# Kernel optimization log

Measured on AMD Instinct MI355X. Metric: run time of the kernel, lower is better.

## Reference

```python
import jax, jax.numpy as jnp
import numpy as np

B, N, F_IN, F_E, H, L = 8, 128, 64, 16, 256, 8
EPS = 1e-5


def _linear_params(key, fan_in, fan_out):
    k1, k2 = jax.random.split(key)
    bound = 1.0 / np.sqrt(fan_in)
    W = jax.random.uniform(k1, (fan_in, fan_out), minval=-bound, maxval=bound, dtype=jnp.float32)
    b = jax.random.uniform(k2, (fan_out,), minval=-bound, maxval=bound, dtype=jnp.float32)
    return W, b


def setup_inputs() -> dict:
    key = jax.random.key(0)
    ks = jax.random.split(key, 16)
    x = jax.random.normal(ks[0], (B, N, F_IN), dtype=jnp.float32)
    adj = jax.random.randint(ks[1], (B, N, N), 0, 2, dtype=jnp.int32)
    edge_attr = jax.random.normal(ks[2], (B, N, N, F_E), dtype=jnp.float32)
    mask = jnp.ones((B, N), dtype=jnp.int32)

    node_W, node_b = _linear_params(ks[3], F_IN, H)
    edge_W, edge_b = _linear_params(ks[4], F_E, H)

    lks = jax.random.split(ks[5], L)
    W1s, b1s, W2s, b2s = [], [], [], []
    for i in range(L):
        a, b_ = jax.random.split(lks[i])
        W1, b1 = _linear_params(a, H, H)
        W2, b2 = _linear_params(b_, H, H)
        W1s.append(W1); b1s.append(b1); W2s.append(W2); b2s.append(b2)
    ln_g = jnp.ones((L, H), dtype=jnp.float32)
    ln_b = jnp.zeros((L, H), dtype=jnp.float32)
    W1 = jnp.stack(W1s); b1 = jnp.stack(b1s)
    W2 = jnp.stack(W2s); b2 = jnp.stack(b2s)

    ro_pW, ro_pb = _linear_params(ks[6], H, H)
    ro_aW, ro_ab = _linear_params(ks[7], H, 1)
    ph_W, ph_b = _linear_params(ks[8], H, 1)

    return dict(x=x, adj=adj, edge_attr=edge_attr, mask=mask,
                node_W=node_W, node_b=node_b, edge_W=edge_W, edge_b=edge_b,
                ln_g=ln_g, ln_b=ln_b, W1=W1, b1=b1, W2=W2, b2=b2,
                ro_pW=ro_pW, ro_pb=ro_pb, ro_aW=ro_aW, ro_ab=ro_ab,
                ph_W=ph_W, ph_b=ph_b)


def _layernorm(x, g, b):
    mu = jnp.mean(x, axis=-1, keepdims=True)
    var = jnp.var(x, axis=-1, keepdims=True)
    return (x - mu) * jax.lax.rsqrt(var + EPS) * g + b


def _gine_forward(x, adjf, edge_attr, maskf,
                  node_W, node_b, edge_W, edge_b,
                  ln_g, ln_b, W1, b1, W2, b2,
                  ro_pW, ro_pb, ro_aW, ro_ab, ph_W, ph_b):
    h = x @ node_W + node_b                      # (B,N,H)
    edge_emb = edge_attr @ edge_W + edge_b       # (B,N,N,H)
    m = maskf[..., None]                         # (B,N,1)

    def layer(h, p):
        g, bln, w1, bb1, w2, bb2 = p
        h = h * m
        h_norm = _layernorm(h, g, bln)
        # message: h_j + e_ij, j indexes axis 2 -> broadcast over axis 1
        m_in = h_norm[:, None, :, :] + edge_emb          # (B,N,N,H)
        mm = jax.nn.relu(jax.nn.relu(m_in @ w1 + bb1) @ w2 + bb2)
        mm = mm * adjf[..., None]
        msg = mm.sum(axis=2)                             # (B,N,H)
        out = (h + msg) * m
        return out, None

    h, _ = jax.lax.scan(layer, h, (ln_g, ln_b, W1, b1, W2, b2))

    # attention readout
    hp = jnp.tanh(h @ ro_pW + ro_pb)
    scores = (hp @ ro_aW).squeeze(-1) + ro_ab            # (B,N)
    scores = jnp.where(maskf > 0, scores, -jnp.inf)
    alpha = jax.nn.softmax(scores, axis=1)
    cnt = jnp.clip(maskf.sum(axis=1, keepdims=True), 1.0, None)
    fallback = jnp.where(maskf > 0, 1.0 / cnt, 0.0)
    alpha = jnp.where(jnp.isnan(alpha), fallback, alpha)
    gvec = (h * alpha[..., None]).sum(axis=1)            # (B,H)
    out = (gvec @ ph_W + ph_b).squeeze(-1)               # (B,)
    return out


def reference(x, adj, edge_attr, mask,
              node_W, node_b, edge_W, edge_b,
              ln_g, ln_b, W1, b1, W2, b2,
              ro_pW, ro_pb, ro_aW, ro_ab, ph_W, ph_b):
    adjf = adj.astype(jnp.float32)
    maskf = mask.astype(jnp.float32)
    return _gine_forward(x, adjf, edge_attr, maskf,
                         node_W, node_b, edge_W, edge_b,
                         ln_g, ln_b, W1, b1, W2, b2,
                         ro_pW, ro_pb, ro_aW, ro_ab, ph_W, ph_b)
```

## Files before the change

kernel.cpp:

```cpp
#include <hip/hip_runtime.h>

typedef float  f32x4  __attribute__((ext_vector_type(4)));
typedef short  bf16x8 __attribute__((ext_vector_type(8)));
typedef unsigned short u16;
typedef unsigned int   u32;

static __device__ __forceinline__ u16 f2bf(float f) {
    u32 u = __float_as_uint(f);
    u += 0x7FFFu + ((u >> 16) & 1u);
    return (u16)(u >> 16);
}



__global__ void k_h0(const float* __restrict__ x, const float* __restrict__ nW,
                     const float* __restrict__ nb, float* __restrict__ h) {
    __shared__ float xr[64];
    int row = blockIdx.x, c = threadIdx.x;
    if (c < 64) xr[c] = x[row * 64 + c];
    __syncthreads();
    float acc = nb[c];
#pragma unroll
    for (int k = 0; k < 64; ++k) acc += xr[k] * nW[k * 256 + c];
    h[row * 256 + c] = acc;
}

__global__ void k_edgefrag(const float* __restrict__ ea, u16* __restrict__ ef) {
    int gid = blockIdx.x * 256 + threadIdx.x;
    int lane = gid & 63, nt = (gid >> 6) & 7, i = (gid >> 9) & 127, b = gid >> 16;
    int j = nt * 16 + (lane & 15), k0 = (lane >> 4) * 8;
    uint4 out = {0u, 0u, 0u, 0u};
    if (k0 < 16) {
        const float* p = ea + (((size_t)(b * 128 + i) * 128 + j) * 16 + k0);
        u16 us[8];
#pragma unroll
        for (int t = 0; t < 8; ++t) us[t] = f2bf(p[t]);
        out.x = (u32)us[0] | ((u32)us[1] << 16);
        out.y = (u32)us[2] | ((u32)us[3] << 16);
        out.z = (u32)us[4] | ((u32)us[5] << 16);
        out.w = (u32)us[6] | ((u32)us[7] << 16);
    }
    ((uint4*)ef)[gid] = out;
}

__global__ void k_wt(const float* __restrict__ W1, const float* __restrict__ W2,
                     u16* __restrict__ w1t, u16* __restrict__ w2t) {
    int gid = blockIdx.x * 256 + threadIdx.x;
    int lane = gid & 63, mt = (gid >> 6) & 15, kt = (gid >> 10) & 7, l = gid >> 13;
    int hh = mt * 16 + (lane & 15), k = kt * 32 + (lane >> 4) * 8;
    u16 a[8], b[8];
#pragma unroll
    for (int t = 0; t < 8; ++t) {
        size_t idx = (size_t)l * 65536 + (size_t)(k + t) * 256 + hh;
        a[t] = f2bf(W1[idx]);
        b[t] = f2bf(W2[idx]);
    }
    uint4 oa, ob;
    oa.x = (u32)a[0] | ((u32)a[1] << 16); oa.y = (u32)a[2] | ((u32)a[3] << 16);
    oa.z = (u32)a[4] | ((u32)a[5] << 16); oa.w = (u32)a[6] | ((u32)a[7] << 16);
    ob.x = (u32)b[0] | ((u32)b[1] << 16); ob.y = (u32)b[2] | ((u32)b[3] << 16);
    ob.z = (u32)b[4] | ((u32)b[5] << 16); ob.w = (u32)b[6] | ((u32)b[7] << 16);
    ((uint4*)w1t)[gid] = oa;
    ((uint4*)w2t)[gid] = ob;
}

__global__ void k_wf1b(const float* __restrict__ eW, const float* __restrict__ eb,
                       const float* __restrict__ W1, const float* __restrict__ b1,
                       u16* __restrict__ wf, float* __restrict__ bias1) {
    __shared__ float eWsT[256 * 16];
    __shared__ float ebS[256];
    int l = blockIdx.x, tid = threadIdx.x;
#pragma unroll
    for (int k = 0; k < 16; ++k) eWsT[tid * 16 + k] = eW[k * 256 + tid];
    ebS[tid] = eb[tid];
    __syncthreads();
    float acc[16];
#pragma unroll
    for (int k = 0; k < 16; ++k) acc[k] = 0.f;
    float bacc = b1[l * 256 + tid];
    const float* w1c = W1 + (size_t)l * 65536 + tid;
    for (int c = 0; c < 256; ++c) {
        float wv = w1c[(size_t)c * 256];
        const f32x4* e = (const f32x4*)&eWsT[c * 16];
#pragma unroll
        for (int q = 0; q < 4; ++q) {
            f32x4 ev = e[q];
#pragma unroll
            for (int t = 0; t < 4; ++t) acc[q * 4 + t] += ev[t] * wv;
        }
        bacc += ebS[c] * wv;
    }
    bias1[l * 256 + tid] = bacc;
    int mt = tid >> 4, lo = tid & 15;
#pragma unroll
    for (int c4 = 0; c4 < 4; ++c4) {
        u16 us[8];
#pragma unroll
        for (int t = 0; t < 8; ++t) {
            int k = c4 * 8 + t;
            us[t] = (k < 16) ? f2bf(acc[k]) : (u16)0;
        }
        uint4 o;
        o.x = (u32)us[0] | ((u32)us[1] << 16);
        o.y = (u32)us[2] | ((u32)us[3] << 16);
        o.z = (u32)us[4] | ((u32)us[5] << 16);
        o.w = (u32)us[6] | ((u32)us[7] << 16);
        ((uint4*)wf)[(size_t)(l * 16 + mt) * 64 + c4 * 16 + lo] = o;
    }
}


__global__ void k_ln(float* __restrict__ h, const int* __restrict__ mask,
                     const float* __restrict__ lng, const float* __restrict__ lnb,
                     u16* __restrict__ hnbf) {
    __shared__ float rs[4], rs2[4];
    int row = blockIdx.x, c = threadIdx.x;
    float mv = (float)mask[row];
    float v = h[row * 256 + c] * mv;
    h[row * 256 + c] = v;
    float s = v, s2 = v * v;
    int w = c >> 6, lane = c & 63;
#pragma unroll
    for (int off = 32; off; off >>= 1) {
        s  += __shfl_xor(s,  off);
        s2 += __shfl_xor(s2, off);
    }
    if (lane == 0) { rs[w] = s; rs2[w] = s2; }
    __syncthreads();
    float S  = rs[0] + rs[1] + rs[2] + rs[3];
    float S2 = rs2[0] + rs2[1] + rs2[2] + rs2[3];
    float mu  = S * (1.f / 256.f);
    float var = S2 * (1.f / 256.f) - mu * mu;
    float rstd = rsqrtf(var + 1e-5f);
    hnbf[row * 256 + c] = f2bf((v - mu) * rstd * lng[c] + lnb[c]);
}

__global__ __launch_bounds__(256) void k_hn1(const u16* __restrict__ w1t,
        const u16* __restrict__ hnbf, const float* __restrict__ bias1,
        float* __restrict__ hn1p, int l) {
    int orig = blockIdx.x;
    int bid = (orig & 7) * 8 + (orig >> 3);
    int b = bid >> 3, q = bid & 7;
    int tid = threadIdx.x, w = tid >> 6, lane = tid & 63;
    int mt = q * 2 + (w >> 1), nb_ = (w & 1) * 4;
    f32x4 bv = *(const f32x4*)(bias1 + l * 256 + mt * 16 + (lane >> 4) * 4);
    f32x4 acc[4];
#pragma unroll
    for (int n = 0; n < 4; ++n) acc[n] = bv;
#pragma unroll
    for (int kt = 0; kt < 8; ++kt) {
        bf16x8 a = *(const bf16x8*)(w1t + ((size_t)((l * 8 + kt) * 16 + mt) * 64 + lane) * 8);
#pragma unroll
        for (int nn = 0; nn < 4; ++nn) {
            int j = (nb_ + nn) * 16 + (lane & 15);
            bf16x8 bt = *(const bf16x8*)(hnbf + ((size_t)(b * 128 + j) * 256 + kt * 32 + (lane >> 4) * 8));
            acc[nn] = __builtin_amdgcn_mfma_f32_16x16x32_bf16(a, bt, acc[nn], 0, 0, 0);
        }
    }
    float* outb = hn1p + (size_t)b * 32768;
#pragma unroll
    for (int nn = 0; nn < 4; ++nn)
        *(f32x4*)(outb + ((size_t)(mt * 8 + nb_ + nn) * 64 + lane) * 4) = acc[nn];
}

__global__ __launch_bounds__(512, 4) void k_msg(
        const u16* __restrict__ wf1t, const u16* __restrict__ ef,
        const u16* __restrict__ w2t,  const float* __restrict__ hn1p,
        const float* __restrict__ b2, const int* __restrict__ adj,
        const int* __restrict__ mask, float* __restrict__ h,
        const float* __restrict__ lngN, const float* __restrict__ lnbN,
        u16* __restrict__ hnbf, int l, int doLN) {

    __shared__ __align__(16) u16  t1S[8 * 8 * 64 * 8];
    __shared__ __align__(16) float adjS[128];
    __shared__ __align__(16) float b2S[256];
    __shared__ __align__(16) float msgS[256];
    __shared__ float rs[8], rs2[8];

    int orig = blockIdx.x;
    int bid = (orig & 7) * 128 + (orig >> 3);
    int b = bid >> 7, i = bid & 127;
    int tid = threadIdx.x, w = tid >> 6, lane = tid & 63;
    int row = b * 128 + i;

    if (tid < 128) adjS[tid] = (float)adj[(size_t)row * 128 + tid];
    if (tid < 256) b2S[tid] = b2[l * 256 + tid];

    const u16* efb = ef + (size_t)row * 4096;
    bf16x8 be[8];
#pragma unroll
    for (int n = 0; n < 8; ++n)
        be[n] = *(const bf16x8*)(efb + (n * 64 + lane) * 8);

    const float* hpb = hn1p + (size_t)b * 32768;
#pragma unroll
    for (int m = 0; m < 2; ++m) {
        int mt = w * 2 + m;
        bf16x8 a = *(const bf16x8*)(wf1t + ((size_t)(l * 16 + mt) * 64 + lane) * 8);
#pragma unroll
        for (int n = 0; n < 8; ++n) {
            f32x4 acc = *(const f32x4*)(hpb + ((size_t)(mt * 8 + n) * 64 + lane) * 4);
            acc = __builtin_amdgcn_mfma_f32_16x16x32_bf16(a, be[n], acc, 0, 0, 0);
            u32 lo = (u32)f2bf(fmaxf(acc[0], 0.f)) | ((u32)f2bf(fmaxf(acc[1], 0.f)) << 16);
            u32 hi = (u32)f2bf(fmaxf(acc[2], 0.f)) | ((u32)f2bf(fmaxf(acc[3], 0.f)) << 16);
            int g    = ((mt & 1) << 1) | (lane >> 5);
            int half = (lane >> 4) & 1;
            uint2 pk; pk.x = lo; pk.y = hi;
            *(uint2*)(t1S + ((size_t)(((mt >> 1) * 8 + n) * 64) + g * 16 + (lane & 15)) * 8 + half * 4) = pk;
        }
    }
    __syncthreads();

    f32x4 acc2[2][8];
#pragma unroll
    for (int m = 0; m < 2; ++m)
#pragma unroll
        for (int n = 0; n < 8; ++n) acc2[m][n] = (f32x4){0.f, 0.f, 0.f, 0.f};

#pragma unroll
    for (int kt = 0; kt < 8; ++kt) {
        bf16x8 a2[2];
#pragma unroll
        for (int m = 0; m < 2; ++m)
            a2[m] = *(const bf16x8*)(w2t + ((size_t)((l * 8 + kt) * 16 + (w * 2 + m)) * 64 + lane) * 8);
#pragma unroll
        for (int n = 0; n < 8; ++n) {
            bf16x8 bt = *(const bf16x8*)(t1S + ((size_t)(kt * 8 + n) * 64 + lane) * 8);
#pragma unroll
            for (int m = 0; m < 2; ++m)
                acc2[m][n] = __builtin_amdgcn_mfma_f32_16x16x32_bf16(a2[m], bt, acc2[m][n], 0, 0, 0);
        }
    }

#pragma unroll
    for (int m = 0; m < 2; ++m) {
        int hb = (w * 2 + m) * 16 + (lane >> 4) * 4;
        f32x4 bv = *(const f32x4*)(&b2S[hb]);
        f32x4 ms = (f32x4){0.f, 0.f, 0.f, 0.f};
#pragma unroll
        for (int n = 0; n < 8; ++n) {
            float aw = adjS[n * 16 + (lane & 15)];
#pragma unroll
            for (int r = 0; r < 4; ++r)
                ms[r] += fmaxf(acc2[m][n][r] + bv[r], 0.f) * aw;
        }
#pragma unroll
        for (int r = 0; r < 4; ++r) {
            ms[r] += __shfl_xor(ms[r], 1);
            ms[r] += __shfl_xor(ms[r], 2);
            ms[r] += __shfl_xor(ms[r], 4);
            ms[r] += __shfl_xor(ms[r], 8);
        }
        if ((lane & 15) == 0) *(f32x4*)(&msgS[hb]) = ms;
    }
    __syncthreads();

    float v = 0.f;
    if (tid < 256) {
        float mv = (float)mask[row];
        v = (h[(size_t)row * 256 + tid] + msgS[tid]) * mv;
        h[(size_t)row * 256 + tid] = v;
    }
    float s = v, s2 = v * v;
#pragma unroll
    for (int off = 32; off; off >>= 1) {
        s  += __shfl_xor(s,  off);
        s2 += __shfl_xor(s2, off);
    }
    if (lane == 0) { rs[w] = s; rs2[w] = s2; }
    __syncthreads();
    if (doLN && tid < 256) {
        float S = 0.f, S2 = 0.f;
#pragma unroll
        for (int t = 0; t < 8; ++t) { S += rs[t]; S2 += rs2[t]; }
        float mu  = S * (1.f / 256.f);
        float var = S2 * (1.f / 256.f) - mu * mu;
        float rstd = rsqrtf(var + 1e-5f);
        hnbf[(size_t)row * 256 + tid] = f2bf((v - mu) * rstd * lngN[tid] + lnbN[tid]);
    }
}


__global__ void k_ro1(const float* __restrict__ h, const float* __restrict__ pW,
                      const float* __restrict__ pb, const float* __restrict__ aW,
                      const float* __restrict__ ab, float* __restrict__ scores) {
    __shared__ float hr[8][256];
    __shared__ float red[4][8];
    int blk = blockIdx.x, b = blk >> 4, g = blk & 15;
    int tid = threadIdx.x;
    size_t base = (size_t)(b * 128 + g * 8) * 256;
#pragma unroll
    for (int t = 0; t < 8; ++t) hr[t][tid] = h[base + t * 256 + tid];
    __syncthreads();
    float facc[8];
    float pbv = pb[tid];
#pragma unroll
    for (int j = 0; j < 8; ++j) facc[j] = pbv;
    for (int k = 0; k < 256; ++k) {
        float wv = pW[(size_t)k * 256 + tid];
#pragma unroll
        for (int j = 0; j < 8; ++j) facc[j] += hr[j][k] * wv;
    }
    float awc = aW[tid];
    int w = tid >> 6, lane = tid & 63;
#pragma unroll
    for (int j = 0; j < 8; ++j) {
        float v = tanhf(facc[j]) * awc;
#pragma unroll
        for (int off = 32; off; off >>= 1) v += __shfl_xor(v, off);
        if (lane == 0) red[w][j] = v;
    }
    __syncthreads();
    if (tid < 8)
        scores[b * 128 + g * 8 + tid] = red[0][tid] + red[1][tid] + red[2][tid] + red[3][tid] + ab[0];
}

__global__ void k_ro2(const float* __restrict__ h, const float* __restrict__ scores,
                      const int* __restrict__ mask, const float* __restrict__ phW,
                      const float* __restrict__ phb, float* __restrict__ out) {
    __shared__ float aS[128];
    __shared__ float rm[4], rc[4], red[4];
    int b = blockIdx.x, tid = threadIdx.x, w = tid >> 6, lane = tid & 63;
    float mv = 0.f, sv = -__builtin_inff();
    if (tid < 128) {
        mv = (float)mask[b * 128 + tid];
        if (mv > 0.f) sv = scores[b * 128 + tid];
    }
    float mx = sv, cs = mv;
#pragma unroll
    for (int off = 32; off; off >>= 1) {
        mx = fmaxf(mx, __shfl_xor(mx, off));
        cs += __shfl_xor(cs, off);
    }
    if (lane == 0) { rm[w] = mx; rc[w] = cs; }
    __syncthreads();
    mx = fmaxf(fmaxf(rm[0], rm[1]), fmaxf(rm[2], rm[3]));
    float cnt = rc[0] + rc[1] + rc[2] + rc[3];
    float e = (tid < 128 && mv > 0.f) ? expf(sv - mx) : 0.f;
    float se = e;
#pragma unroll
    for (int off = 32; off; off >>= 1) se += __shfl_xor(se, off);
    if (lane == 0) red[w] = se;
    __syncthreads();
    float S = red[0] + red[1] + red[2] + red[3];
    if (tid < 128) {
        float a;
        if (S > 0.f) a = e / S;
        else         a = (mv > 0.f) ? 1.f / fmaxf(cnt, 1.f) : 0.f;
        aS[tid] = a;
    }
    __syncthreads();
    float g = 0.f;
    const float* hb = h + (size_t)b * 128 * 256;
    for (int n = 0; n < 128; ++n) g += aS[n] * hb[(size_t)n * 256 + tid];
    float p = g * phW[tid];
#pragma unroll
    for (int off = 32; off; off >>= 1) p += __shfl_xor(p, off);
    __syncthreads();
    if (lane == 0) red[w] = p;
    __syncthreads();
    if (tid == 0) out[b] = red[0] + red[1] + red[2] + red[3] + phb[0];
}

extern "C" void kernel_launch(void* const* d_in, const int* in_sizes, int n_in,
                              void* d_out, int out_size, void* d_ws, size_t ws_size,
                              hipStream_t stream) {
    const float* x    = (const float*)d_in[0];
    const int*   adj  = (const int*)  d_in[1];
    const float* ea   = (const float*)d_in[2];
    const int*   mask = (const int*)  d_in[3];
    const float* nW   = (const float*)d_in[4];
    const float* nb   = (const float*)d_in[5];
    const float* eW   = (const float*)d_in[6];
    const float* eb   = (const float*)d_in[7];
    const float* lng  = (const float*)d_in[8];
    const float* lnb  = (const float*)d_in[9];
    const float* W1   = (const float*)d_in[10];
    const float* b1   = (const float*)d_in[11];
    const float* W2   = (const float*)d_in[12];
    const float* b2   = (const float*)d_in[13];
    const float* ropW = (const float*)d_in[14];
    const float* ropb = (const float*)d_in[15];
    const float* roaW = (const float*)d_in[16];
    const float* roab = (const float*)d_in[17];
    const float* phW  = (const float*)d_in[18];
    const float* phb  = (const float*)d_in[19];
    float* out = (float*)d_out;

    char* p = (char*)d_ws;
    auto alloc = [&](size_t bytes) { char* r = p; p += (bytes + 255) & ~(size_t)255; return r; };
    float* h     = (float*)alloc((size_t)8 * 128 * 256 * 4);
    u16*   hnbf  = (u16*)  alloc((size_t)8 * 128 * 256 * 2);
    float* hn1p  = (float*)alloc((size_t)8 * 32768 * 4);
    u16*   ef    = (u16*)  alloc((size_t)8 * 128 * 4096 * 2);
    u16*   wf1t  = (u16*)  alloc((size_t)8 * 16 * 64 * 8 * 2);
    u16*   w1t   = (u16*)  alloc((size_t)8 * 8 * 16 * 64 * 8 * 2);
    u16*   w2t   = (u16*)  alloc((size_t)8 * 8 * 16 * 64 * 8 * 2);
    float* bias1 = (float*)alloc((size_t)8 * 256 * 4);
    float* scores= (float*)alloc((size_t)1024 * 4);

    k_h0      <<<1024, 256, 0, stream>>>(x, nW, nb, h);
    k_edgefrag<<<2048, 256, 0, stream>>>(ea, ef);
    k_wt      <<<256,  256, 0, stream>>>(W1, W2, w1t, w2t);
    k_wf1b    <<<8,    256, 0, stream>>>(eW, eb, W1, b1, wf1t, bias1);
    k_ln      <<<1024, 256, 0, stream>>>(h, mask, lng, lnb, hnbf);

    for (int l = 0; l < 8; ++l) {
        k_hn1<<<64,   256, 0, stream>>>(w1t, hnbf, bias1, hn1p, l);
        int doLN = (l < 7) ? 1 : 0;
        int ln_next = (l < 7) ? (l + 1) : l;
        k_msg<<<1024, 512, 0, stream>>>(wf1t, ef, w2t, hn1p, b2, adj, mask, h,
                                        lng + ln_next * 256, lnb + ln_next * 256,
                                        hnbf, l, doLN);
    }

    k_ro1<<<128, 256, 0, stream>>>(h, ropW, ropb, roaW, roab, scores);
    k_ro2<<<8,   256, 0, stream>>>(h, scores, mask, phW, phb, out);
}
```

Baseline: 396.3 us.

## Compact adjacency neighbors and skip MLP work on absent edges

After: 355.8 us. -10.2%, faster.

```diff
diff --git a/kernel.cpp b/kernel.cpp
--- a/kernel.cpp
+++ b/kernel.cpp
@@ -13,16 +13,36 @@
 
 
 
-__global__ void k_h0(const float* __restrict__ x, const float* __restrict__ nW,
-                     const float* __restrict__ nb, float* __restrict__ h) {
+__global__ void k_h0ln(const float* __restrict__ x, const float* __restrict__ nW,
+                       const float* __restrict__ nb, const int* __restrict__ mask,
+                       const float* __restrict__ lng, const float* __restrict__ lnb,
+                       float* __restrict__ h, u16* __restrict__ hnbf) {
     __shared__ float xr[64];
+    __shared__ float rs[4], rs2[4];
     int row = blockIdx.x, c = threadIdx.x;
     if (c < 64) xr[c] = x[row * 64 + c];
     __syncthreads();
     float acc = nb[c];
 #pragma unroll
     for (int k = 0; k < 64; ++k) acc += xr[k] * nW[k * 256 + c];
-    h[row * 256 + c] = acc;
+    float mv = (float)mask[row];
+    float v = acc * mv;
+    h[row * 256 + c] = v;
+    float s = v, s2 = v * v;
+    int w = c >> 6, lane = c & 63;
+#pragma unroll
+    for (int off = 32; off; off >>= 1) {
+        s  += __shfl_xor(s,  off);
+        s2 += __shfl_xor(s2, off);
+    }
+    if (lane == 0) { rs[w] = s; rs2[w] = s2; }
+    __syncthreads();
+    float S  = rs[0] + rs[1] + rs[2] + rs[3];
+    float S2 = rs2[0] + rs2[1] + rs2[2] + rs2[3];
+    float mu  = S * (1.f / 256.f);
+    float var = S2 * (1.f / 256.f) - mu * mu;
+    float rstd = rsqrtf(var + 1e-5f);
+    hnbf[row * 256 + c] = f2bf((v - mu) * rstd * lng[c] + lnb[c]);
 }
 
 __global__ void k_edgefrag(const float* __restrict__ ea, u16* __restrict__ ef) {
@@ -110,57 +130,27 @@
 }
 
 
-__global__ void k_ln(float* __restrict__ h, const int* __restrict__ mask,
-                     const float* __restrict__ lng, const float* __restrict__ lnb,
-                     u16* __restrict__ hnbf) {
-    __shared__ float rs[4], rs2[4];
-    int row = blockIdx.x, c = threadIdx.x;
-    float mv = (float)mask[row];
-    float v = h[row * 256 + c] * mv;
-    h[row * 256 + c] = v;
-    float s = v, s2 = v * v;
-    int w = c >> 6, lane = c & 63;
-#pragma unroll
-    for (int off = 32; off; off >>= 1) {
-        s  += __shfl_xor(s,  off);
-        s2 += __shfl_xor(s2, off);
-    }
-    if (lane == 0) { rs[w] = s; rs2[w] = s2; }
-    __syncthreads();
-    float S  = rs[0] + rs[1] + rs[2] + rs[3];
-    float S2 = rs2[0] + rs2[1] + rs2[2] + rs2[3];
-    float mu  = S * (1.f / 256.f);
-    float var = S2 * (1.f / 256.f) - mu * mu;
-    float rstd = rsqrtf(var + 1e-5f);
-    hnbf[row * 256 + c] = f2bf((v - mu) * rstd * lng[c] + lnb[c]);
-}
-
 __global__ __launch_bounds__(256) void k_hn1(const u16* __restrict__ w1t,
         const u16* __restrict__ hnbf, const float* __restrict__ bias1,
         float* __restrict__ hn1p, int l) {
     int orig = blockIdx.x;
-    int bid = (orig & 7) * 8 + (orig >> 3);
-    int b = bid >> 3, q = bid & 7;
+    int bid = (orig & 7) * 16 + (orig >> 3);
+    int b = bid >> 4, mt = bid & 15;
     int tid = threadIdx.x, w = tid >> 6, lane = tid & 63;
-    int mt = q * 2 + (w >> 1), nb_ = (w & 1) * 4;
     f32x4 bv = *(const f32x4*)(bias1 + l * 256 + mt * 16 + (lane >> 4) * 4);
-    f32x4 acc[4];
-#pragma unroll
-    for (int n = 0; n < 4; ++n) acc[n] = bv;
+    f32x4 acc0 = bv, acc1 = bv;
+    int j0 = (w * 2) * 16 + (lane & 15), j1 = j0 + 16;
 #pragma unroll
     for (int kt = 0; kt < 8; ++kt) {
         bf16x8 a = *(const bf16x8*)(w1t + ((size_t)((l * 8 + kt) * 16 + mt) * 64 + lane) * 8);
-#pragma unroll
-        for (int nn = 0; nn < 4; ++nn) {
-            int j = (nb_ + nn) * 16 + (lane & 15);
-            bf16x8 bt = *(const bf16x8*)(hnbf + ((size_t)(b * 128 + j) * 256 + kt * 32 + (lane >> 4) * 8));
-            acc[nn] = __builtin_amdgcn_mfma_f32_16x16x32_bf16(a, bt, acc[nn], 0, 0, 0);
-        }
+        bf16x8 bt0 = *(const bf16x8*)(hnbf + ((size_t)(b * 128 + j0) * 256 + kt * 32 + (lane >> 4) * 8));
+        bf16x8 bt1 = *(const bf16x8*)(hnbf + ((size_t)(b * 128 + j1) * 256 + kt * 32 + (lane >> 4) * 8));
+        acc0 = __builtin_amdgcn_mfma_f32_16x16x32_bf16(a, bt0, acc0, 0, 0, 0);
+        acc1 = __builtin_amdgcn_mfma_f32_16x16x32_bf16(a, bt1, acc1, 0, 0, 0);
     }
     float* outb = hn1p + (size_t)b * 32768;
-#pragma unroll
-    for (int nn = 0; nn < 4; ++nn)
-        *(f32x4*)(outb + ((size_t)(mt * 8 + nb_ + nn) * 64 + lane) * 4) = acc[nn];
+    *(f32x4*)(outb + ((size_t)(mt * 8 + w * 2) * 64 + lane) * 4)     = acc0;
+    *(f32x4*)(outb + ((size_t)(mt * 8 + w * 2 + 1) * 64 + lane) * 4) = acc1;
 }
 
 __global__ __launch_bounds__(512, 4) void k_msg(
@@ -172,9 +162,11 @@
         u16* __restrict__ hnbf, int l, int doLN) {
 
     __shared__ __align__(16) u16  t1S[8 * 8 * 64 * 8];
-    __shared__ __align__(16) float adjS[128];
     __shared__ __align__(16) float b2S[256];
     __shared__ __align__(16) float msgS[256];
+    __shared__ int listS[128];
+    __shared__ int flagS[128];
+    __shared__ int cntS;
     __shared__ float rs[8], rs2[8];
 
     int orig = blockIdx.x;
@@ -183,75 +175,92 @@
     int tid = threadIdx.x, w = tid >> 6, lane = tid & 63;
     int row = b * 128 + i;
 
-    if (tid < 128) adjS[tid] = (float)adj[(size_t)row * 128 + tid];
+    if (tid < 128) { flagS[tid] = adj[(size_t)row * 128 + tid]; listS[tid] = 0; }
     if (tid < 256) b2S[tid] = b2[l * 256 + tid];
-
-    const u16* efb = ef + (size_t)row * 4096;
-    bf16x8 be[8];
-#pragma unroll
-    for (int n = 0; n < 8; ++n)
-        be[n] = *(const bf16x8*)(efb + (n * 64 + lane) * 8);
-
+    __syncthreads();
+
+    if (w == 0) {
+        int f0 = flagS[lane], f1 = flagS[64 + lane];
+        unsigned long long m0 = __ballot(f0 != 0);
+        unsigned long long m1 = __ballot(f1 != 0);
+        unsigned long long lt = (1ull << lane) - 1ull;
+        int c0 = __popcll(m0);
+        if (f0) listS[__popcll(m0 & lt)] = lane;
+        if (f1) listS[c0 + __popcll(m1 & lt)] = 64 + lane;
+        if (lane == 0) cntS = c0 + __popcll(m1);
+    }
+    __syncthreads();
+    int cnt = cntS;
+    int NT = (cnt + 15) >> 4;
+
+    const u16*  efb = ef + (size_t)row * 4096;
     const float* hpb = hn1p + (size_t)b * 32768;
-#pragma unroll
-    for (int m = 0; m < 2; ++m) {
-        int mt = w * 2 + m;
-        bf16x8 a = *(const bf16x8*)(wf1t + ((size_t)(l * 16 + mt) * 64 + lane) * 8);
-#pragma unroll
-        for (int n = 0; n < 8; ++n) {
-            f32x4 acc = *(const f32x4*)(hpb + ((size_t)(mt * 8 + n) * 64 + lane) * 4);
-            acc = __builtin_amdgcn_mfma_f32_16x16x32_bf16(a, be[n], acc, 0, 0, 0);
+    int mt0 = w * 2, mt1 = w * 2 + 1;
+    bf16x8 aG0 = *(const bf16x8*)(wf1t + ((size_t)(l * 16 + mt0) * 64 + lane) * 8);
+    bf16x8 aG1 = *(const bf16x8*)(wf1t + ((size_t)(l * 16 + mt1) * 64 + lane) * 8);
+    for (int n = 0; n < NT; ++n) {
+        int j = listS[n * 16 + (lane & 15)];
+        int jo = (j >> 4) * 64 + (lane & 48) + (j & 15);
+        bf16x8 be = *(const bf16x8*)(efb + (size_t)jo * 8);
+        {
+            f32x4 ci = *(const f32x4*)(hpb + ((size_t)(mt0 * 8) * 64 + jo) * 4);
+            f32x4 acc = __builtin_amdgcn_mfma_f32_16x16x32_bf16(aG0, be, ci, 0, 0, 0);
             u32 lo = (u32)f2bf(fmaxf(acc[0], 0.f)) | ((u32)f2bf(fmaxf(acc[1], 0.f)) << 16);
             u32 hi = (u32)f2bf(fmaxf(acc[2], 0.f)) | ((u32)f2bf(fmaxf(acc[3], 0.f)) << 16);
-            int g    = ((mt & 1) << 1) | (lane >> 5);
-            int half = (lane >> 4) & 1;
+            int g = ((mt0 & 1) << 1) | (lane >> 5), half = (lane >> 4) & 1;
             uint2 pk; pk.x = lo; pk.y = hi;
-            *(uint2*)(t1S + ((size_t)(((mt >> 1) * 8 + n) * 64) + g * 16 + (lane & 15)) * 8 + half * 4) = pk;
-        }
-    }
-    __syncthreads();
-
-    f32x4 acc2[2][8];
-#pragma unroll
-    for (int m = 0; m < 2; ++m)
-#pragma unroll
-        for (int n = 0; n < 8; ++n) acc2[m][n] = (f32x4){0.f, 0.f, 0.f, 0.f};
-
+            *(uint2*)(t1S + ((size_t)((w * 8 + n) * 64) + g * 16 + (lane & 15)) * 8 + half * 4) = pk;
+        }
+        {
+            f32x4 ci = *(const f32x4*)(hpb + ((size_t)(mt1 * 8) * 64 + jo) * 4);
+            f32x4 acc = __builtin_amdgcn_mfma_f32_16x16x32_bf16(aG1, be, ci, 0, 0, 0);
+            u32 lo = (u32)f2bf(fmaxf(acc[0], 0.f)) | ((u32)f2bf(fmaxf(acc[1], 0.f)) << 16);
+            u32 hi = (u32)f2bf(fmaxf(acc[2], 0.f)) | ((u32)f2bf(fmaxf(acc[3], 0.f)) << 16);
+            int g = ((mt1 & 1) << 1) | (lane >> 5), half = (lane >> 4) & 1;
+            uint2 pk; pk.x = lo; pk.y = hi;
+            *(uint2*)(t1S + ((size_t)((w * 8 + n) * 64) + g * 16 + (lane & 15)) * 8 + half * 4) = pk;
+        }
+    }
+    __syncthreads();
+
+    bf16x8 a2[8][2];
 #pragma unroll
     for (int kt = 0; kt < 8; ++kt) {
-        bf16x8 a2[2];
-#pragma unroll
-        for (int m = 0; m < 2; ++m)
-            a2[m] = *(const bf16x8*)(w2t + ((size_t)((l * 8 + kt) * 16 + (w * 2 + m)) * 64 + lane) * 8);
-#pragma unroll
-        for (int n = 0; n < 8; ++n) {
+        a2[kt][0] = *(const bf16x8*)(w2t + ((size_t)((l * 8 + kt) * 16 + mt0) * 64 + lane) * 8);
+        a2[kt][1] = *(const bf16x8*)(w2t + ((size_t)((l * 8 + kt) * 16 + mt1) * 64 + lane) * 8);
+    }
+    int hb0 = mt0 * 16 + (lane >> 4) * 4;
+    int hb1 = mt1 * 16 + (lane >> 4) * 4;
+    f32x4 bv0 = *(const f32x4*)(&b2S[hb0]);
+    f32x4 bv1 = *(const f32x4*)(&b2S[hb1]);
+    f32x4 ms0 = (f32x4){0.f, 0.f, 0.f, 0.f};
+    f32x4 ms1 = (f32x4){0.f, 0.f, 0.f, 0.f};
+    for (int n = 0; n < NT; ++n) {
+        f32x4 acc0 = (f32x4){0.f, 0.f, 0.f, 0.f};
+        f32x4 acc1 = (f32x4){0.f, 0.f, 0.f, 0.f};
+#pragma unroll
+        for (int kt = 0; kt < 8; ++kt) {
             bf16x8 bt = *(const bf16x8*)(t1S + ((size_t)(kt * 8 + n) * 64 + lane) * 8);
-#pragma unroll
-            for (int m = 0; m < 2; ++m)
-                acc2[m][n] = __builtin_amdgcn_mfma_f32_16x16x32_bf16(a2[m], bt, acc2[m][n], 0, 0, 0);
-        }
-    }
-
-#pragma unroll
-    for (int m = 0; m < 2; ++m) {
-        int hb = (w * 2 + m) * 16 + (lane >> 4) * 4;
-        f32x4 bv = *(const f32x4*)(&b2S[hb]);
-        f32x4 ms = (f32x4){0.f, 0.f, 0.f, 0.f};
-#pragma unroll
-        for (int n = 0; n < 8; ++n) {
-            float aw = adjS[n * 16 + (lane & 15)];
-#pragma unroll
-            for (int r = 0; r < 4; ++r)
-                ms[r] += fmaxf(acc2[m][n][r] + bv[r], 0.f) * aw;
-        }
+            acc0 = __builtin_amdgcn_mfma_f32_16x16x32_bf16(a2[kt][0], bt, acc0, 0, 0, 0);
+            acc1 = __builtin_amdgcn_mfma_f32_16x16x32_bf16(a2[kt][1], bt, acc1, 0, 0, 0);
+        }
+        float aw = (n * 16 + (lane & 15)) < cnt ? 1.f : 0.f;
 #pragma unroll
         for (int r = 0; r < 4; ++r) {
-            ms[r] += __shfl_xor(ms[r], 1);
-            ms[r] += __shfl_xor(ms[r], 2);
-            ms[r] += __shfl_xor(ms[r], 4);
-            ms[r] += __shfl_xor(ms[r], 8);
-        }
-        if ((lane & 15) == 0) *(f32x4*)(&msgS[hb]) = ms;
+            ms0[r] += fmaxf(acc0[r] + bv0[r], 0.f) * aw;
+            ms1[r] += fmaxf(acc1[r] + bv1[r], 0.f) * aw;
+        }
+    }
+#pragma unroll
+    for (int r = 0; r < 4; ++r) {
+        ms0[r] += __shfl_xor(ms0[r], 1); ms1[r] += __shfl_xor(ms1[r], 1);
+        ms0[r] += __shfl_xor(ms0[r], 2); ms1[r] += __shfl_xor(ms1[r], 2);
+        ms0[r] += __shfl_xor(ms0[r], 4); ms1[r] += __shfl_xor(ms1[r], 4);
+        ms0[r] += __shfl_xor(ms0[r], 8); ms1[r] += __shfl_xor(ms1[r], 8);
+    }
+    if ((lane & 15) == 0) {
+        *(f32x4*)(&msgS[hb0]) = ms0;
+        *(f32x4*)(&msgS[hb1]) = ms1;
     }
     __syncthreads();
 
@@ -399,14 +408,13 @@
     float* bias1 = (float*)alloc((size_t)8 * 256 * 4);
     float* scores= (float*)alloc((size_t)1024 * 4);
 
-    k_h0      <<<1024, 256, 0, stream>>>(x, nW, nb, h);
+    k_h0ln    <<<1024, 256, 0, stream>>>(x, nW, nb, mask, lng, lnb, h, hnbf);
     k_edgefrag<<<2048, 256, 0, stream>>>(ea, ef);
     k_wt      <<<256,  256, 0, stream>>>(W1, W2, w1t, w2t);
     k_wf1b    <<<8,    256, 0, stream>>>(eW, eb, W1, b1, wf1t, bias1);
-    k_ln      <<<1024, 256, 0, stream>>>(h, mask, lng, lnb, hnbf);
 
     for (int l = 0; l < 8; ++l) {
-        k_hn1<<<64,   256, 0, stream>>>(w1t, hnbf, bias1, hn1p, l);
+        k_hn1<<<128,  256, 0, stream>>>(w1t, hnbf, bias1, hn1p, l);
         int doLN = (l < 7) ? 1 : 0;
         int ln_next = (l < 7) ? (l + 1) : l;
         k_msg<<<1024, 512, 0, stream>>>(wf1t, ef, w2t, hn1p, b2, adj, mask, h,
```
